# Kernel tuning notes

Measured on AMD Instinct MI355X. Metric: run time of the kernel, lower is better.

The kernel has to match this reference:

```python
import jax, jax.numpy as jnp
import numpy as np

MASK_VALUE = -1000000.0  # matches sequence_mask fill in the torch source


def setup_inputs() -> dict:
    key = jax.random.key(0)
    k1, k2, k3, k4 = jax.random.split(key, 4)
    B, Lq, Lk, D = 64, 1024, 1024, 64
    return {
        "queries": jax.random.normal(k1, (B, Lq, D), dtype=jnp.float32),
        "keys": jax.random.normal(k2, (B, Lk, D), dtype=jnp.float32),
        "values": jax.random.normal(k3, (B, Lk, D), dtype=jnp.float32),
        "valid_lens": jax.random.randint(k4, (B,), 1, Lk + 1, dtype=jnp.int64),
    }


def reference(queries, keys, values, valid_lens):
    # queries: [B, Lq, D], keys/values: [B, Lk, D], valid_lens: [B]
    d = queries.shape[-1]
    qk = jnp.einsum("bqd,bkd->bqk", queries, keys) / jnp.sqrt(jnp.asarray(d, queries.dtype))
    # sequence_mask: positions >= valid_len are set to -1e6 before softmax.
    # valid_lens is per-batch-row, broadcast over queries (repeat_interleave in torch).
    kpos = jnp.arange(keys.shape[1])  # [Lk]
    mask = kpos[None, None, :] < valid_lens[:, None, None]  # [B, 1, Lk] -> broadcast over q
    qk = jnp.where(mask, qk, jnp.asarray(MASK_VALUE, qk.dtype))
    attn = jax.nn.softmax(qk, axis=-1)
    return jnp.einsum("bqk,bkd->bqd", attn, values)
```

## Files before the change

### kernel.cpp

```cpp
#include <hip/hip_runtime.h>
#include <hip/hip_bf16.h>


#define NB    64
#define LQ    1024
#define LK    1024
#define DH    64
#define KVT   64
#define QT    128
#define NITEMS (NB * (LQ / QT))
#define NEGF  1.0e30f
#define SC2   0.18033688011112042f
#define THR   8.0f

typedef __attribute__((ext_vector_type(8))) short    bf8;
typedef __attribute__((ext_vector_type(8))) ushort   u16x8;
typedef __attribute__((ext_vector_type(4))) ushort   u16x4;
typedef __attribute__((ext_vector_type(4))) float    f4;

__device__ __forceinline__ ushort2 cvt2(float a, float b) {
    float2 f; f.x = a; f.y = b;
    __hip_bfloat162 h = __float22bfloat162_rn(f);
    union { __hip_bfloat162 h2; ushort2 u2; } u;
    u.h2 = h;
    return u.u2;
}
__device__ __forceinline__ int swz16(int row, int colbyte) {
    return row * 128 + ((((colbyte >> 4) ^ (row & 7)) << 4) | (colbyte & 15));
}
__device__ __forceinline__ float fm3(float a, float b, float c) {
    return fmaxf(fmaxf(a, b), c);
}

__global__ __launch_bounds__(512, 4)
void attn_v21(const float* __restrict__ Q, const float* __restrict__ K,
              const float* __restrict__ V, const int* __restrict__ VL,
              float* __restrict__ O) {
    __shared__ ushort KsB[2][KVT * DH];
    __shared__ ushort VtB[2][DH * KVT];
    __shared__ ushort sched[NB];

    const int tid = threadIdx.x;
    const int wid = tid >> 6, l = tid & 63, g = l >> 4, a = l & 15;

    if (tid < NB) {
        const int ntb = (VL[tid] + KVT - 1) >> 6;
        int r = 0;
        for (int j = 0; j < NB; ++j) {
            const int ntj = (VL[j] + KVT - 1) >> 6;
            r += (int)((ntj > ntb) | ((ntj == ntb) & (j < tid)));
        }
        sched[r] = (ushort)tid;
    }
    __syncthreads();
    const int xcd   = blockIdx.x & 7;
    const int slot  = blockIdx.x >> 3;
    const int qtile = slot & 7;
    const int st    = slot >> 3;
    const int rank  = xcd + ((st < 4) ? st : (11 - st)) * 8;
    const int b     = sched[rank];
    const int qbase = qtile * QT;
    const int valid = VL[b];
    const int nt = (valid + KVT - 1) >> 6;

    int off8[8];
    #pragma unroll
    for (int n = 0; n < 4; ++n)
        #pragma unroll
        for (int kblk = 0; kblk < 2; ++kblk)
            off8[n * 2 + kblk] = swz16(n * 16 + a, kblk * 64 + g * 16);

    const float* Qr = Q + ((size_t)b * LQ + qbase + wid * 16 + a) * DH;
    bf8 qa[2];
    #pragma unroll
    for (int kblk = 0; kblk < 2; ++kblk) {
        f4 x = *(const f4*)(Qr + kblk * 32 + g * 8);
        f4 y = *(const f4*)(Qr + kblk * 32 + g * 8 + 4);
        ushort2 c0 = cvt2(x[0] * SC2, x[1] * SC2), c1 = cvt2(x[2] * SC2, x[3] * SC2);
        ushort2 c2 = cvt2(y[0] * SC2, y[1] * SC2), c3 = cvt2(y[2] * SC2, y[3] * SC2);
        qa[kblk][0] = (short)c0.x; qa[kblk][1] = (short)c0.y;
        qa[kblk][2] = (short)c1.x; qa[kblk][3] = (short)c1.y;
        qa[kblk][4] = (short)c2.x; qa[kblk][5] = (short)c2.y;
        qa[kblk][6] = (short)c3.x; qa[kblk][7] = (short)c3.y;
    }
    const bf8 ones = {0x3F80, 0x3F80, 0x3F80, 0x3F80,
                      0x3F80, 0x3F80, 0x3F80, 0x3F80};

    const int  rtid  = tid & 255;
    const bool vrole = (wid < 4);
    const int srow = rtid >> 3, sslot = rtid & 7;
    const int vkp  = rtid >> 4, vj = rtid & 15;
    const int prow = (srow & 3) | ((srow & 24) >> 1) | ((srow & 4) << 2);
    const f4* Kb4 = (const f4*)(K + (size_t)b * LK * DH);
    const f4* Vb4 = (const f4*)(V + (size_t)b * LK * DH);

    f4 r0, r1, r2, r3;
    auto load_kv = [&](int k0) {
        if (vrole) {
            r0 = Vb4[(k0 + 4 * vkp + 0) * 16 + vj];
            r1 = Vb4[(k0 + 4 * vkp + 1) * 16 + vj];
            r2 = Vb4[(k0 + 4 * vkp + 2) * 16 + vj];
            r3 = Vb4[(k0 + 4 * vkp + 3) * 16 + vj];
        } else {
            r0 = Kb4[(k0 + srow) * 16 + sslot * 2];
            r1 = Kb4[(k0 + srow) * 16 + sslot * 2 + 1];
            r2 = Kb4[(k0 + srow + 32) * 16 + sslot * 2];
            r3 = Kb4[(k0 + srow + 32) * 16 + sslot * 2 + 1];
        }
    };
    auto store_kv = [&](int bs) {
        if (vrole) {
            char* vd = (char*)&VtB[bs][0];
            #pragma unroll
            for (int c = 0; c < 4; ++c) {
                ushort2 a01 = cvt2(r0[c], r1[c]), a23 = cvt2(r2[c], r3[c]);
                u16x4 p = {a01.x, a01.y, a23.x, a23.y};
                *(u16x4*)(vd + swz16(4 * vj + c, vkp * 8)) = p;
            }
        } else {
            char* kd = (char*)&KsB[bs][0];
            {
                ushort2 c0 = cvt2(r0[0], r0[1]), c1 = cvt2(r0[2], r0[3]);
                ushort2 c2 = cvt2(r1[0], r1[1]), c3 = cvt2(r1[2], r1[3]);
                u16x8 w = {c0.x, c0.y, c1.x, c1.y, c2.x, c2.y, c3.x, c3.y};
                *(u16x8*)(kd + swz16(prow, sslot * 16)) = w;
            }
            {
                ushort2 c0 = cvt2(r2[0], r2[1]), c1 = cvt2(r2[2], r2[3]);
                ushort2 c2 = cvt2(r3[0], r3[1]), c3 = cvt2(r3[2], r3[3]);
                u16x8 w = {c0.x, c0.y, c1.x, c1.y, c2.x, c2.y, c3.x, c3.y};
                *(u16x8*)(kd + swz16(prow + 32, sslot * 16)) = w;
            }
        }
    };

    f4 oacc[4];
    #pragma unroll
    for (int n = 0; n < 4; ++n) oacc[n] = f4{0.f, 0.f, 0.f, 0.f};
    f4 lacc = f4{0.f, 0.f, 0.f, 0.f};
    float m_run = -NEGF;

    auto tile_iter = [&](int t, const int bs) {
        __syncthreads();
        if (t + 1 < nt) load_kv((t + 1) * KVT);
        __builtin_amdgcn_sched_barrier(0);

        const char* kd = (const char*)&KsB[bs][0];
        f4 sacc[4];
        #pragma unroll
        for (int n = 0; n < 4; ++n) sacc[n] = f4{0.f, 0.f, 0.f, 0.f};
        __builtin_amdgcn_s_setprio(1);
        #pragma unroll
        for (int n = 0; n < 4; ++n)
            #pragma unroll
            for (int kblk = 0; kblk < 2; ++kblk) {
                bf8 kb = *(const bf8*)(kd + off8[n * 2 + kblk]);
                sacc[n] = __builtin_amdgcn_mfma_f32_16x16x32_bf16(
                    kb, qa[kblk], sacc[n], 0, 0, 0);
            }
        __builtin_amdgcn_s_setprio(0);

        const int kmax = valid - t * KVT;
        if (kmax < KVT) {
            #pragma unroll
            for (int n = 0; n < 4; ++n)
                #pragma unroll
                for (int r = 0; r < 4; ++r)
                    if (32 * (n >> 1) + 4 * (n & 1) + 8 * g + r >= kmax)
                        sacc[n][r] = -NEGF;
        }

        float t0 = fm3(sacc[0][0], sacc[0][1], sacc[0][2]);
        float t1 = fm3(sacc[0][3], sacc[1][0], sacc[1][1]);
        float t2 = fm3(sacc[1][2], sacc[1][3], sacc[2][0]);
        float t3 = fm3(sacc[2][1], sacc[2][2], sacc[2][3]);
        float t4 = fm3(sacc[3][0], sacc[3][1], sacc[3][2]);
        float tm = fm3(fm3(t0, t1, t2), fm3(t3, t4, sacc[3][3]),
                       -NEGF);
        tm = fmaxf(tm, __shfl_xor(tm, 16));
        tm = fmaxf(tm, __shfl_xor(tm, 32));

        float rs_ = 1.0f;
        const bool skip = __all(tm <= m_run + THR);
        if (!skip) {
            const float mnew = fmaxf(m_run, tm);
            rs_ = __builtin_exp2f(m_run - mnew);
            m_run = mnew;
        }

        float p[4][4];
        #pragma unroll
        for (int n = 0; n < 4; ++n)
            #pragma unroll
            for (int r = 0; r < 4; ++r)
                p[n][r] = __builtin_exp2f(sacc[n][r] - m_run);

        if (!skip) {
            float rr[4];
            #pragma unroll
            for (int r = 0; r < 4; ++r) rr[r] = __shfl(rs_, 4 * g + r);
            #pragma unroll
            for (int n = 0; n < 4; ++n)
                #pragma unroll
                for (int r = 0; r < 4; ++r) oacc[n][r] *= rr[r];
            #pragma unroll
            for (int r = 0; r < 4; ++r) lacc[r] *= rr[r];
        }

        const char* vd = (const char*)&VtB[bs][0];
        __builtin_amdgcn_s_setprio(1);
        #pragma unroll
        for (int kblk = 0; kblk < 2; ++kblk) {
            ushort2 w0 = cvt2(p[2 * kblk][0], p[2 * kblk][1]);
            ushort2 w1 = cvt2(p[2 * kblk][2], p[2 * kblk][3]);
            ushort2 w2 = cvt2(p[2 * kblk + 1][0], p[2 * kblk + 1][1]);
            ushort2 w3 = cvt2(p[2 * kblk + 1][2], p[2 * kblk + 1][3]);
            bf8 pa = {(short)w0.x, (short)w0.y, (short)w1.x, (short)w1.y,
                      (short)w2.x, (short)w2.y, (short)w3.x, (short)w3.y};
            #pragma unroll
            for (int n = 0; n < 4; ++n) {
                bf8 vb_ = *(const bf8*)(vd + off8[n * 2 + kblk]);
                oacc[n] = __builtin_amdgcn_mfma_f32_16x16x32_bf16(
                    pa, vb_, oacc[n], 0, 0, 0);
            }
            lacc = __builtin_amdgcn_mfma_f32_16x16x32_bf16(pa, ones, lacc, 0, 0, 0);
        }
        __builtin_amdgcn_s_setprio(0);

        if (t + 1 < nt) store_kv(bs ^ 1);
    };

    load_kv(0);
    store_kv(0);
    for (int t = 0; t < nt; t += 2) {
        tile_iter(t, 0);
        if (t + 1 < nt) tile_iter(t + 1, 1);
    }

    float iv[4];
    #pragma unroll
    for (int r = 0; r < 4; ++r) iv[r] = 1.0f / lacc[r];
    float* Ob = O + ((size_t)b * LQ + qbase + wid * 16) * DH;
    #pragma unroll
    for (int n = 0; n < 4; ++n)
        #pragma unroll
        for (int r = 0; r < 4; ++r)
            Ob[(size_t)(4 * g + r) * DH + 16 * n + a] = oacc[n][r] * iv[r];
}

extern "C" void kernel_launch(void* const* d_in, const int* in_sizes, int n_in,
                              void* d_out, int out_size, void* d_ws, size_t ws_size,
                              hipStream_t stream) {
    const float* Q  = (const float*)d_in[0];
    const float* K  = (const float*)d_in[1];
    const float* V  = (const float*)d_in[2];
    const int*   VL = (const int*)d_in[3];
    float* O = (float*)d_out;

    attn_v21<<<NITEMS, 512, 0, stream>>>(Q, K, V, VL, O);
}
```

Baseline: 33.06 us.

## Split KV tiles across two warp groups per block and merge partial softmax

Doubles the block to 1024 threads, with two groups of 8 waves each processing half of the KV tiles for the same 128 query rows using separate double-buffered LDS. At the end, group 1 writes its partial O, row sums and running max to shared memory, and group 0 rescales and combines them before writing the output. This halves the serial KV-loop length per block to reduce per-block latency and tail imbalance. In exchange it adds a merge step, more barriers across all 16 waves, and higher register/LDS pressure per CU.

```diff
diff --git a/kernel.cpp b/kernel.cpp
--- a/kernel.cpp
+++ b/kernel.cpp
@@ -32,16 +32,19 @@
     return fmaxf(fmaxf(a, b), c);
 }
 
-__global__ __launch_bounds__(512, 4)
-void attn_v21(const float* __restrict__ Q, const float* __restrict__ K,
+__global__ __launch_bounds__(1024, 8)
+void attn_v24(const float* __restrict__ Q, const float* __restrict__ K,
               const float* __restrict__ V, const int* __restrict__ VL,
               float* __restrict__ O) {
-    __shared__ ushort KsB[2][KVT * DH];
-    __shared__ ushort VtB[2][DH * KVT];
+    __shared__ ushort KsB[2][2][KVT * DH];
+    __shared__ ushort VtB[2][2][DH * KVT];
     __shared__ ushort sched[NB];
 
     const int tid = threadIdx.x;
-    const int wid = tid >> 6, l = tid & 63, g = l >> 4, a = l & 15;
+    const int wid = tid >> 6;
+    const int grp = wid >> 3;
+    const int gw  = wid & 7;
+    const int l = tid & 63, g = l >> 4, a = l & 15;
 
     if (tid < NB) {
         const int ntb = (VL[tid] + KVT - 1) >> 6;
@@ -62,6 +65,9 @@
     const int qbase = qtile * QT;
     const int valid = VL[b];
     const int nt = (valid + KVT - 1) >> 6;
+    const int hA   = (nt + 1) >> 1;
+    const int myN  = grp ? (nt - hA) : hA;
+    const int tbase = grp ? hA : 0;
 
     int off8[8];
     #pragma unroll
@@ -70,7 +76,7 @@
         for (int kblk = 0; kblk < 2; ++kblk)
             off8[n * 2 + kblk] = swz16(n * 16 + a, kblk * 64 + g * 16);
 
-    const float* Qr = Q + ((size_t)b * LQ + qbase + wid * 16 + a) * DH;
+    const float* Qr = Q + ((size_t)b * LQ + qbase + gw * 16 + a) * DH;
     bf8 qa[2];
     #pragma unroll
     for (int kblk = 0; kblk < 2; ++kblk) {
@@ -86,13 +92,16 @@
     const bf8 ones = {0x3F80, 0x3F80, 0x3F80, 0x3F80,
                       0x3F80, 0x3F80, 0x3F80, 0x3F80};
 
-    const int  rtid  = tid & 255;
-    const bool vrole = (wid < 4);
+    const int  ltid  = tid & 511;
+    const int  rtid  = ltid & 255;
+    const bool vrole = (gw < 4);
     const int srow = rtid >> 3, sslot = rtid & 7;
     const int vkp  = rtid >> 4, vj = rtid & 15;
     const int prow = (srow & 3) | ((srow & 24) >> 1) | ((srow & 4) << 2);
     const f4* Kb4 = (const f4*)(K + (size_t)b * LK * DH);
     const f4* Vb4 = (const f4*)(V + (size_t)b * LK * DH);
+    char* kbase[2] = {(char*)&KsB[grp][0][0], (char*)&KsB[grp][1][0]};
+    char* vbase[2] = {(char*)&VtB[grp][0][0], (char*)&VtB[grp][1][0]};
 
     f4 r0, r1, r2, r3;
     auto load_kv = [&](int k0) {
@@ -110,7 +119,7 @@
     };
     auto store_kv = [&](int bs) {
         if (vrole) {
-            char* vd = (char*)&VtB[bs][0];
+            char* vd = vbase[bs];
             #pragma unroll
             for (int c = 0; c < 4; ++c) {
                 ushort2 a01 = cvt2(r0[c], r1[c]), a23 = cvt2(r2[c], r3[c]);
@@ -118,7 +127,7 @@
                 *(u16x4*)(vd + swz16(4 * vj + c, vkp * 8)) = p;
             }
         } else {
-            char* kd = (char*)&KsB[bs][0];
+            char* kd = kbase[bs];
             {
                 ushort2 c0 = cvt2(r0[0], r0[1]), c1 = cvt2(r0[2], r0[3]);
                 ushort2 c2 = cvt2(r1[0], r1[1]), c3 = cvt2(r1[2], r1[3]);
@@ -140,112 +149,141 @@
     f4 lacc = f4{0.f, 0.f, 0.f, 0.f};
     float m_run = -NEGF;
 
-    auto tile_iter = [&](int t, const int bs) {
+    if (myN > 0) { load_kv(tbase * KVT); store_kv(0); }
+
+    auto tile_iter = [&](int u, const int bs) {
         __syncthreads();
-        if (t + 1 < nt) load_kv((t + 1) * KVT);
+        if (u + 1 < myN) load_kv((tbase + u + 1) * KVT);
         __builtin_amdgcn_sched_barrier(0);
-
-        const char* kd = (const char*)&KsB[bs][0];
-        f4 sacc[4];
-        #pragma unroll
-        for (int n = 0; n < 4; ++n) sacc[n] = f4{0.f, 0.f, 0.f, 0.f};
-        __builtin_amdgcn_s_setprio(1);
+        if (u < myN) {
+            const char* kd = kbase[bs];
+            f4 sacc[4];
+            #pragma unroll
+            for (int n = 0; n < 4; ++n) sacc[n] = f4{0.f, 0.f, 0.f, 0.f};
+            __builtin_amdgcn_s_setprio(1);
+            #pragma unroll
+            for (int n = 0; n < 4; ++n)
+                #pragma unroll
+                for (int kblk = 0; kblk < 2; ++kblk) {
+                    bf8 kb = *(const bf8*)(kd + off8[n * 2 + kblk]);
+                    sacc[n] = __builtin_amdgcn_mfma_f32_16x16x32_bf16(
+                        kb, qa[kblk], sacc[n], 0, 0, 0);
+                }
+            __builtin_amdgcn_s_setprio(0);
+
+            const int kmax = valid - (tbase + u) * KVT;
+            if (kmax < KVT) {
+                #pragma unroll
+                for (int n = 0; n < 4; ++n)
+                    #pragma unroll
+                    for (int r = 0; r < 4; ++r)
+                        if (32 * (n >> 1) + 4 * (n & 1) + 8 * g + r >= kmax)
+                            sacc[n][r] = -NEGF;
+            }
+
+            float t0 = fm3(sacc[0][0], sacc[0][1], sacc[0][2]);
+            float t1 = fm3(sacc[0][3], sacc[1][0], sacc[1][1]);
+            float t2 = fm3(sacc[1][2], sacc[1][3], sacc[2][0]);
+            float t3 = fm3(sacc[2][1], sacc[2][2], sacc[2][3]);
+            float t4 = fm3(sacc[3][0], sacc[3][1], sacc[3][2]);
+            float tm = fmaxf(fm3(t0, t1, t2), fm3(t3, t4, sacc[3][3]));
+            tm = fmaxf(tm, __shfl_xor(tm, 16));
+            tm = fmaxf(tm, __shfl_xor(tm, 32));
+
+            float rs_ = 1.0f;
+            const bool skip = __all(tm <= m_run + THR);
+            if (!skip) {
+                const float mnew = fmaxf(m_run, tm);
+                rs_ = __builtin_exp2f(m_run - mnew);
+                m_run = mnew;
+            }
+
+            float p[4][4];
+            #pragma unroll
+            for (int n = 0; n < 4; ++n)
+                #pragma unroll
+                for (int r = 0; r < 4; ++r)
+                    p[n][r] = __builtin_exp2f(sacc[n][r] - m_run);
+
+            if (!skip) {
+                float rr[4];
+                #pragma unroll
+                for (int r = 0; r < 4; ++r) rr[r] = __shfl(rs_, 4 * g + r);
+                #pragma unroll
+                for (int n = 0; n < 4; ++n)
+                    #pragma unroll
+                    for (int r = 0; r < 4; ++r) oacc[n][r] *= rr[r];
+                #pragma unroll
+                for (int r = 0; r < 4; ++r) lacc[r] *= rr[r];
+            }
+
+            const char* vd = vbase[bs];
+            __builtin_amdgcn_s_setprio(1);
+            #pragma unroll
+            for (int kblk = 0; kblk < 2; ++kblk) {
+                ushort2 w0 = cvt2(p[2 * kblk][0], p[2 * kblk][1]);
+                ushort2 w1 = cvt2(p[2 * kblk][2], p[2 * kblk][3]);
+                ushort2 w2 = cvt2(p[2 * kblk + 1][0], p[2 * kblk + 1][1]);
+                ushort2 w3 = cvt2(p[2 * kblk + 1][2], p[2 * kblk + 1][3]);
+                bf8 pa = {(short)w0.x, (short)w0.y, (short)w1.x, (short)w1.y,
+                          (short)w2.x, (short)w2.y, (short)w3.x, (short)w3.y};
+                #pragma unroll
+                for (int n = 0; n < 4; ++n) {
+                    bf8 vb_ = *(const bf8*)(vd + off8[n * 2 + kblk]);
+                    oacc[n] = __builtin_amdgcn_mfma_f32_16x16x32_bf16(
+                        pa, vb_, oacc[n], 0, 0, 0);
+                }
+                lacc = __builtin_amdgcn_mfma_f32_16x16x32_bf16(pa, ones, lacc, 0, 0, 0);
+            }
+            __builtin_amdgcn_s_setprio(0);
+        }
+        if (u + 1 < myN) store_kv(bs ^ 1);
+    };
+
+    for (int u = 0; u < hA; u += 2) {
+        tile_iter(u, 0);
+        if (u + 1 < hA) tile_iter(u + 1, 1);
+    }
+
+    __syncthreads();
+    float* Oex = (float*)&KsB[0][0][0];
+    float* lex = (float*)&VtB[0][0][0];
+    float* mex = lex + 128;
+    if (grp == 1) {
         #pragma unroll
         for (int n = 0; n < 4; ++n)
             #pragma unroll
-            for (int kblk = 0; kblk < 2; ++kblk) {
-                bf8 kb = *(const bf8*)(kd + off8[n * 2 + kblk]);
-                sacc[n] = __builtin_amdgcn_mfma_f32_16x16x32_bf16(
-                    kb, qa[kblk], sacc[n], 0, 0, 0);
-            }
-        __builtin_amdgcn_s_setprio(0);
-
-        const int kmax = valid - t * KVT;
-        if (kmax < KVT) {
-            #pragma unroll
-            for (int n = 0; n < 4; ++n)
-                #pragma unroll
-                for (int r = 0; r < 4; ++r)
-                    if (32 * (n >> 1) + 4 * (n & 1) + 8 * g + r >= kmax)
-                        sacc[n][r] = -NEGF;
-        }
-
-        float t0 = fm3(sacc[0][0], sacc[0][1], sacc[0][2]);
-        float t1 = fm3(sacc[0][3], sacc[1][0], sacc[1][1]);
-        float t2 = fm3(sacc[1][2], sacc[1][3], sacc[2][0]);
-        float t3 = fm3(sacc[2][1], sacc[2][2], sacc[2][3]);
-        float t4 = fm3(sacc[3][0], sacc[3][1], sacc[3][2]);
-        float tm = fm3(fm3(t0, t1, t2), fm3(t3, t4, sacc[3][3]),
-                       -NEGF);
-        tm = fmaxf(tm, __shfl_xor(tm, 16));
-        tm = fmaxf(tm, __shfl_xor(tm, 32));
-
-        float rs_ = 1.0f;
-        const bool skip = __all(tm <= m_run + THR);
-        if (!skip) {
-            const float mnew = fmaxf(m_run, tm);
-            rs_ = __builtin_exp2f(m_run - mnew);
-            m_run = mnew;
-        }
-
-        float p[4][4];
+            for (int r = 0; r < 4; ++r)
+                Oex[((gw * 4 + n) * 16 + (4 * g + r)) * 16 + a] = oacc[n][r];
+        if (a == 0) {
+            #pragma unroll
+            for (int r = 0; r < 4; ++r) lex[gw * 16 + 4 * g + r] = lacc[r];
+        }
+        if (g == 0) mex[gw * 16 + a] = m_run;
+    }
+    __syncthreads();
+    if (grp == 0) {
+        float w0[4], w1[4], iv[4];
+        #pragma unroll
+        for (int r = 0; r < 4; ++r) {
+            const float m0r = __shfl(m_run, 4 * g + r);
+            const float m1r = mex[gw * 16 + 4 * g + r];
+            const float l1r = lex[gw * 16 + 4 * g + r];
+            const float mm  = fmaxf(m0r, m1r);
+            w0[r] = __builtin_exp2f(m0r - mm);
+            w1[r] = __builtin_exp2f(m1r - mm);
+            iv[r] = 1.0f / (lacc[r] * w0[r] + l1r * w1[r]);
+        }
+        float* Ob = O + ((size_t)b * LQ + qbase + gw * 16) * DH;
         #pragma unroll
         for (int n = 0; n < 4; ++n)
             #pragma unroll
-            for (int r = 0; r < 4; ++r)
-                p[n][r] = __builtin_exp2f(sacc[n][r] - m_run);
-
-        if (!skip) {
-            float rr[4];
-            #pragma unroll
-            for (int r = 0; r < 4; ++r) rr[r] = __shfl(rs_, 4 * g + r);
-            #pragma unroll
-            for (int n = 0; n < 4; ++n)
-                #pragma unroll
-                for (int r = 0; r < 4; ++r) oacc[n][r] *= rr[r];
-            #pragma unroll
-            for (int r = 0; r < 4; ++r) lacc[r] *= rr[r];
-        }
-
-        const char* vd = (const char*)&VtB[bs][0];
-        __builtin_amdgcn_s_setprio(1);
-        #pragma unroll
-        for (int kblk = 0; kblk < 2; ++kblk) {
-            ushort2 w0 = cvt2(p[2 * kblk][0], p[2 * kblk][1]);
-            ushort2 w1 = cvt2(p[2 * kblk][2], p[2 * kblk][3]);
-            ushort2 w2 = cvt2(p[2 * kblk + 1][0], p[2 * kblk + 1][1]);
-            ushort2 w3 = cvt2(p[2 * kblk + 1][2], p[2 * kblk + 1][3]);
-            bf8 pa = {(short)w0.x, (short)w0.y, (short)w1.x, (short)w1.y,
-                      (short)w2.x, (short)w2.y, (short)w3.x, (short)w3.y};
-            #pragma unroll
-            for (int n = 0; n < 4; ++n) {
-                bf8 vb_ = *(const bf8*)(vd + off8[n * 2 + kblk]);
-                oacc[n] = __builtin_amdgcn_mfma_f32_16x16x32_bf16(
-                    pa, vb_, oacc[n], 0, 0, 0);
-            }
-            lacc = __builtin_amdgcn_mfma_f32_16x16x32_bf16(pa, ones, lacc, 0, 0, 0);
-        }
-        __builtin_amdgcn_s_setprio(0);
-
-        if (t + 1 < nt) store_kv(bs ^ 1);
-    };
-
-    load_kv(0);
-    store_kv(0);
-    for (int t = 0; t < nt; t += 2) {
-        tile_iter(t, 0);
-        if (t + 1 < nt) tile_iter(t + 1, 1);
-    }
-
-    float iv[4];
-    #pragma unroll
-    for (int r = 0; r < 4; ++r) iv[r] = 1.0f / lacc[r];
-    float* Ob = O + ((size_t)b * LQ + qbase + wid * 16) * DH;
-    #pragma unroll
-    for (int n = 0; n < 4; ++n)
-        #pragma unroll
-        for (int r = 0; r < 4; ++r)
-            Ob[(size_t)(4 * g + r) * DH + 16 * n + a] = oacc[n][r] * iv[r];
+            for (int r = 0; r < 4; ++r) {
+                const float o1 = Oex[((gw * 4 + n) * 16 + (4 * g + r)) * 16 + a];
+                Ob[(size_t)(4 * g + r) * DH + 16 * n + a] =
+                    (oacc[n][r] * w0[r] + o1 * w1[r]) * iv[r];
+            }
+    }
 }
 
 extern "C" void kernel_launch(void* const* d_in, const int* in_sizes, int n_in,
@@ -257,5 +295,5 @@
     const int*   VL = (const int*)d_in[3];
     float* O = (float*)d_out;
 
-    attn_v21<<<NITEMS, 512, 0, stream>>>(Q, K, V, VL, O);
-}
+    attn_v24<<<NITEMS, 1024, 0, stream>>>(Q, K, V, VL, O);
+}
```

After: 103.2 us. 3.12x slower.
